# Kernel tuning notes

Measured on AMD Instinct MI355X. Metric: run time of the kernel, lower is better.

Reference implementation:

```python
import jax, jax.numpy as jnp
import numpy as np

B, S, T = 256, 1024, 64

def setup_inputs() -> dict:
    key = jax.random.key(0)
    k1, k2, k3, k4, k5 = jax.random.split(key, 5)
    emissions = jax.random.normal(k1, (B, S, T), dtype=jnp.float32)
    tags = jax.random.randint(k2, (B, S), 0, T, dtype=jnp.int64)
    mask = jnp.ones((B, S), dtype=jnp.int32)
    transitions = jax.random.normal(k3, (T, T), dtype=jnp.float32) * 0.1
    start_transitions = jax.random.normal(k4, (T,), dtype=jnp.float32) * 0.1
    end_transitions = jax.random.normal(k5, (T,), dtype=jnp.float32) * 0.1
    return {"emissions": emissions, "tags": tags, "mask": mask,
            "transitions": transitions, "start_transitions": start_transitions,
            "end_transitions": end_transitions}


def _gold_score(emissions, tags, maskf, transitions, start_transitions, end_transitions):
    # emission score at each gold tag: [B, S]
    emit = jnp.take_along_axis(emissions, tags[:, :, None], axis=2)[:, :, 0]
    # transition score between consecutive gold tags: [B, S-1]
    trans = transitions[tags[:, :-1], tags[:, 1:]]
    score = start_transitions[tags[:, 0]] + emit[:, 0]
    score = score + jnp.sum((trans + emit[:, 1:]) * maskf[:, 1:], axis=1)
    last_pos = maskf.astype(jnp.int32).sum(axis=1) - 1           # [B]
    last_tags = jnp.take_along_axis(tags, last_pos[:, None], axis=1)[:, 0]
    return score + end_transitions[last_tags]


def _log_partition(emissions, maskf, transitions, start_transitions, end_transitions):
    alpha0 = start_transitions[None, :] + emissions[:, 0]        # [B, T]

    def step(alpha, xs):
        emit_t, m_t = xs                                         # [B, T], [B]
        # scores[b, i, j] = alpha[b, i] + transitions[i, j] + emit_t[b, j]
        scores = alpha[:, :, None] + transitions[None, :, :] + emit_t[:, None, :]
        new_alpha = jax.nn.logsumexp(scores, axis=1)             # [B, T]
        alpha = jnp.where(m_t[:, None] > 0, new_alpha, alpha)
        return alpha, None

    xs = (jnp.swapaxes(emissions[:, 1:], 0, 1), jnp.swapaxes(maskf[:, 1:], 0, 1))
    alpha, _ = jax.lax.scan(step, alpha0, xs)
    return jax.nn.logsumexp(alpha + end_transitions[None, :], axis=1)  # [B]


def reference(emissions, tags, mask, transitions, start_transitions, end_transitions):
    maskf = mask.astype(emissions.dtype)
    log_Z = _log_partition(emissions, maskf, transitions, start_transitions, end_transitions)
    score = _gold_score(emissions, tags, maskf, transitions, start_transitions, end_transitions)
    return jnp.mean(log_Z - score)
```

## Files before the change

### kernel.cpp

```cpp
#include <hip/hip_runtime.h>

#define Bn 256
#define Sn 1024
#define Tn 64
#define NCH 16
#define BURN 64
#define SLAB 4
#define CROW 72
#define MROW 129
#define LN2 0.69314718055994531f
#define L7LN2 4.8520302639196169f

typedef __attribute__((ext_vector_type(8))) short short8;
typedef __attribute__((ext_vector_type(4))) float f32x4;

__device__ __forceinline__ unsigned short f2bf_rne(float f) {
  unsigned u = __float_as_uint(f);
  u = (u + 0x7fffu + ((u >> 16) & 1u)) >> 16;
  return (unsigned short)u;
}
__device__ __forceinline__ unsigned pk2(float hi, float lo) {
  return __builtin_amdgcn_perm(__float_as_uint(hi), __float_as_uint(lo), 0x07060302);
}
__device__ __forceinline__ unsigned pke(float a, float b) {
  return (unsigned)f2bf_rne(__expf(a - L7LN2)) |
         ((unsigned)f2bf_rne(__expf(b - L7LN2)) << 16);
}
__device__ __forceinline__ short8 cat4(uint2 a, uint2 b) {
  union { unsigned u[4]; short8 s; } x;
  x.u[0] = a.x; x.u[1] = a.y; x.u[2] = b.x; x.u[3] = b.y;
  return x.s;
}
__device__ __forceinline__ void gl_lds4(const void* src, void* dst) {
  __builtin_amdgcn_global_load_lds(
      (const __attribute__((address_space(1))) void*)src,
      (__attribute__((address_space(3))) void*)dst, 4, 0, 0);
}

__global__ __launch_bounds__(256, 1) void crf_scan(
    const float* __restrict__ em, const int* __restrict__ tags,
    const int* __restrict__ mask, const float* __restrict__ trans,
    const float* __restrict__ startt, const float* __restrict__ endt,
    float* __restrict__ wsL, float* __restrict__ wsGold,
    int* __restrict__ wsM, float* __restrict__ wsSE, float* __restrict__ wsA,
    int* __restrict__ cnt, float* __restrict__ out) {
  const int g = blockIdx.x & 15;
  const int c = blockIdx.x >> 4;
  const int Wc = (c == 0) ? 0 : BURN;
  const int Lc = (c == NCH - 1) ? 63 : 64;
  const int TOT = Wc + Lc;
  const int NSLAB = (TOT + SLAB - 1) / SLAB;
  const int t0 = 64 * c + 1;
  const int tstart = t0 - Wc;
  const int tid = threadIdx.x;
  const int wid = tid >> 6;
  const int lane = tid & 63;
  const int m = lane & 15;
  const int q = lane >> 4;
  const int mrow = 8 * (m >> 2) + (m & 3);

  __shared__ __align__(16) short convS[2][SLAB * 16 * CROW];
  __shared__ int maskL[16 * MROW];
  __shared__ int lastF;
  __shared__ float eend[64];
  __shared__ float rsum[4];

  short8 a00, a01, a10, a11, a20, a21, a30, a31;
  uint2 st0, st1, st2, st3;
  float Slog = 0.f;
  int K = 0, NL = 0;
  const f32x4 zero4 = {0.f, 0.f, 0.f, 0.f};

  const int mm_ = lane & 15, seg_ = lane >> 4;
  const int base_ = (seg_ >> 1) * 32 + (seg_ & 1) * 8;
  const size_t rowoff = (size_t)(16 * g + mm_) * Sn;
  const int ua = (wid == 1) ? 0 : 2;
  float4 A0, A1, A2, A3, A4, A5, A6, A7;
  float4 B0, B1, B2, B3, B4, B5, B6, B7;
  float4 C0, C1, C2, C3, C4, C5, C6, C7;
  float4 D0, D1, D2, D3, D4, D5, D6, D7;

#define LOADS(P, s) do { if ((s) < NSLAB) { \
    int ta_ = tstart + 4 * (s) + ua;  int tb_ = ta_ + 1; \
    ta_ = min(ta_, Sn - 1);  tb_ = min(tb_, Sn - 1);    \
    const float* pa_ = em + (rowoff + ta_) * 64 + seg_ * 16; \
    const float* pb_ = em + (rowoff + tb_) * 64 + seg_ * 16; \
    P##0 = *(const float4*)(pa_);      P##1 = *(const float4*)(pa_ + 4); \
    P##2 = *(const float4*)(pa_ + 8);  P##3 = *(const float4*)(pa_ + 12); \
    P##4 = *(const float4*)(pb_);      P##5 = *(const float4*)(pb_ + 4); \
    P##6 = *(const float4*)(pb_ + 8);  P##7 = *(const float4*)(pb_ + 12); } } while (0)

#define CONVW(P, s) do { if ((s) < NSLAB) { \
    short* cb_ = convS[(s) & 1]; \
    uint4 o0_, o1_; \
    o0_.x = pke((P##0).x, (P##0).y); o0_.y = pke((P##0).z, (P##0).w); \
    o1_.x = pke((P##1).x, (P##1).y); o1_.y = pke((P##1).z, (P##1).w); \
    o0_.z = pke((P##2).x, (P##2).y); o0_.w = pke((P##2).z, (P##2).w); \
    o1_.z = pke((P##3).x, (P##3).y); o1_.w = pke((P##3).z, (P##3).w); \
    short* cw_ = cb_ + (ua * 16 + mm_) * CROW + base_; \
    *(uint4*)(cw_) = o0_;  *(uint4*)(cw_ + 16) = o1_; \
    o0_.x = pke((P##4).x, (P##4).y); o0_.y = pke((P##4).z, (P##4).w); \
    o1_.x = pke((P##5).x, (P##5).y); o1_.y = pke((P##5).z, (P##5).w); \
    o0_.z = pke((P##6).x, (P##6).y); o0_.w = pke((P##6).z, (P##6).w); \
    o1_.z = pke((P##7).x, (P##7).y); o1_.w = pke((P##7).z, (P##7).w); \
    cw_ = cb_ + ((ua + 1) * 16 + mm_) * CROW + base_; \
    *(uint4*)(cw_) = o0_;  *(uint4*)(cw_ + 16) = o1_; } } while (0)

  if (wid == 0) {
#define LOADA(tm, kc, dst) { \
    _Pragma("unroll") for (int jj = 0; jj < 8; ++jj) { \
      int kk = kc * 32 + q * 8 + jj; \
      dst[jj] = (short)f2bf_rne(__expf(trans[kk * Tn + (32 * ((tm) >> 1) + 4 * ((tm) & 1) + mrow)])); \
    } }
    LOADA(0, 0, a00) LOADA(0, 1, a01) LOADA(1, 0, a10) LOADA(1, 1, a11)
    LOADA(2, 0, a20) LOADA(2, 1, a21) LOADA(3, 0, a30) LOADA(3, 1, a31)
#undef LOADA
    if (c == 0) {
#define INIT0(off, ss) { \
      float4 sv = *(const float4*)(startt + (off)); \
      float4 ev = *(const float4*)(em + (size_t)(16 * g + m) * Sn * Tn + (off)); \
      ss.x = (unsigned)f2bf_rne(__expf(sv.x + ev.x)) | \
             ((unsigned)f2bf_rne(__expf(sv.y + ev.y)) << 16); \
      ss.y = (unsigned)f2bf_rne(__expf(sv.z + ev.z)) | \
             ((unsigned)f2bf_rne(__expf(sv.w + ev.w)) << 16); }
      INIT0(8 * q, st0) INIT0(8 * q + 4, st1)
      INIT0(32 + 8 * q, st2) INIT0(36 + 8 * q, st3)
#undef INIT0
    } else {
      st0.x = 0x3F803F80u; st0.y = 0x3F803F80u; st1 = st0; st2 = st0; st3 = st0;
    }
  } else if (wid == 3) {
    for (int mm = 0; mm < 16; ++mm) {
      gl_lds4(mask + (size_t)(16 * g + mm) * Sn + tstart + lane,
              (void*)(maskL + mm * MROW));
      bool special = (c == NCH - 1) && (g == 15) && (mm == 15);
      if (!special)
        gl_lds4(mask + (size_t)(16 * g + mm) * Sn + tstart + 64 + lane,
                (void*)(maskL + mm * MROW + 64));
    }
    {
      const int bm = 16 * g + m;
      const int* tg = tags + (size_t)bm * Sn;
      const int* mkb = mask + (size_t)bm * Sn;
      const float* emb = em + (size_t)bm * Sn * Tn;
      float acc = 0.f;
      int cntg = 0;
      #pragma unroll 4
      for (int i = 0; i < 16; ++i) {
        int t = t0 + q + 4 * i;
        bool ok = t < t0 + Lc;
        int ts = ok ? t : t0;
        int mv = mkb[ts];
        int tp = tg[ts - 1], tc = tg[ts];
        float w = trans[tp * Tn + tc] + emb[(size_t)ts * Tn + tc];
        acc += (ok && mv) ? w : 0.f;
        cntg += ok ? mv : 0;
      }
      acc += __shfl_xor(acc, 16); acc += __shfl_xor(acc, 32);
      cntg += __shfl_xor(cntg, 16); cntg += __shfl_xor(cntg, 32);
      if (q == 0) { wsGold[c * 256 + bm] = acc; wsM[c * 256 + bm] = cntg; }
    }
    if (c == NCH - 1 && g == 15) {
      int t = tstart + 64 + lane;
      if (t < Sn) maskL[15 * MROW + 64 + lane] = mask[(size_t)255 * Sn + t];
    }
    asm volatile("s_waitcnt vmcnt(0) lgkmcnt(0)" ::: "memory");
  } else {
    LOADS(A, 0);
    LOADS(B, 1);
    LOADS(C, 2);
    LOADS(D, 3);
    CONVW(A, 0);
    asm volatile("s_waitcnt lgkmcnt(0)" ::: "memory");
  }
  __builtin_amdgcn_s_barrier();
  asm volatile("" ::: "memory");

#define UNP(ss, x0, x1, x2, x3) \
  x0 = __uint_as_float(ss.x << 16); x1 = __uint_as_float(ss.x & 0xffff0000u); \
  x2 = __uint_as_float(ss.y << 16); x3 = __uint_as_float(ss.y & 0xffff0000u);

  auto renorm = [&](int ttz) {
    float x00, x01, x02, x03, x10, x11, x12, x13;
    float x20, x21, x22, x23, x30, x31, x32, x33;
    UNP(st0, x00, x01, x02, x03) UNP(st1, x10, x11, x12, x13)
    UNP(st2, x20, x21, x22, x23) UNP(st3, x30, x31, x32, x33)
    float sm = (((x00 + x01) + (x02 + x03)) + ((x10 + x11) + (x12 + x13)))
             + (((x20 + x21) + (x22 + x23)) + ((x30 + x31) + (x32 + x33)));
    sm += __shfl_xor(sm, 16); sm += __shfl_xor(sm, 32);
    if (c != 0 && ttz == BURN) { Slog = __logf(sm); K = 0; NL = 0; }
    int k = 127 - (int)((__float_as_uint(sm) >> 23) & 255u);
    float fk = __uint_as_float((unsigned)(127 + k) << 23);
    x00 *= fk; x01 *= fk; x02 *= fk; x03 *= fk;
    x10 *= fk; x11 *= fk; x12 *= fk; x13 *= fk;
    x20 *= fk; x21 *= fk; x22 *= fk; x23 *= fk;
    x30 *= fk; x31 *= fk; x32 *= fk; x33 *= fk;
    st0.x = pk2(x01, x00); st0.y = pk2(x03, x02);
    st1.x = pk2(x11, x10); st1.y = pk2(x13, x12);
    st2.x = pk2(x21, x20); st2.y = pk2(x23, x22);
    st3.x = pk2(x31, x30); st3.y = pk2(x33, x32);
    K += k;
  };

  auto scan_step = [&](const short* ep, int tt) {
    uint2 eu0 = *(const uint2*)(ep + 0 + 4 * q);
    uint2 eu1 = *(const uint2*)(ep + 16 + 4 * q);
    uint2 eu2 = *(const uint2*)(ep + 32 + 4 * q);
    uint2 eu3 = *(const uint2*)(ep + 48 + 4 * q);
    int mv = maskL[m * MROW + tt];
    short8 b0 = cat4(st0, st1);
    short8 b1 = cat4(st2, st3);
    f32x4 d0 = __builtin_amdgcn_mfma_f32_16x16x32_bf16(a00, b0, zero4, 0, 0, 0);
    f32x4 d1 = __builtin_amdgcn_mfma_f32_16x16x32_bf16(a10, b0, zero4, 0, 0, 0);
    f32x4 d2 = __builtin_amdgcn_mfma_f32_16x16x32_bf16(a20, b0, zero4, 0, 0, 0);
    f32x4 d3 = __builtin_amdgcn_mfma_f32_16x16x32_bf16(a30, b0, zero4, 0, 0, 0);
    d0 = __builtin_amdgcn_mfma_f32_16x16x32_bf16(a01, b1, d0, 0, 0, 0);
    d1 = __builtin_amdgcn_mfma_f32_16x16x32_bf16(a11, b1, d1, 0, 0, 0);
    d2 = __builtin_amdgcn_mfma_f32_16x16x32_bf16(a21, b1, d2, 0, 0, 0);
    d3 = __builtin_amdgcn_mfma_f32_16x16x32_bf16(a31, b1, d3, 0, 0, 0);
    const bool live = (mv != 0);
#define EPI(dd, eu, ss) { \
    float e0 = __uint_as_float(eu.x << 16); \
    float e1 = __uint_as_float(eu.x & 0xffff0000u); \
    float e2 = __uint_as_float(eu.y << 16); \
    float e3 = __uint_as_float(eu.y & 0xffff0000u); \
    unsigned nx = pk2(dd[1] * e1, dd[0] * e0); \
    unsigned ny = pk2(dd[3] * e3, dd[2] * e2); \
    ss.x = live ? nx : ss.x; \
    ss.y = live ? ny : ss.y; }
    EPI(d0, eu0, st0) EPI(d1, eu1, st1) EPI(d2, eu2, st2) EPI(d3, eu3, st3)
#undef EPI
    NL += (live && tt >= Wc) ? 1 : 0;
  };

  const int RT = (TOT - 4) >> 2;
  for (int r = 0; r < NSLAB; ++r) {
    if (wid == 0) {
      if ((r & 1) == 0) renorm(4 * r);
      const short* cbase = convS[r & 1];
      if (r < RT) {
        #pragma unroll
        for (int u = 0; u < SLAB; ++u)
          scan_step(cbase + (u * 16 + m) * CROW, 4 * r + u);
      } else {
        #pragma unroll
        for (int u = 0; u < SLAB; ++u)
          if (4 * r + u < TOT)
            scan_step(cbase + (u * 16 + m) * CROW, 4 * r + u);
      }
    } else if (wid == 1 || wid == 2) {
      switch (r & 3) {
        case 0: LOADS(A, r + 4); CONVW(B, r + 1); break;
        case 1: LOADS(B, r + 4); CONVW(C, r + 1); break;
        case 2: LOADS(C, r + 4); CONVW(D, r + 1); break;
        default: LOADS(D, r + 4); CONVW(A, r + 1); break;
      }
      asm volatile("s_waitcnt lgkmcnt(0)" ::: "memory");
    }
    __builtin_amdgcn_s_barrier();
    asm volatile("" ::: "memory");
  }
#undef LOADS
#undef CONVW

  if (wid == 0) {
    float x00, x01, x02, x03, x10, x11, x12, x13;
    float x20, x21, x22, x23, x30, x31, x32, x33;
    UNP(st0, x00, x01, x02, x03) UNP(st1, x10, x11, x12, x13)
    UNP(st2, x20, x21, x22, x23) UNP(st3, x30, x31, x32, x33)
    float sm = (((x00 + x01) + (x02 + x03)) + ((x10 + x11) + (x12 + x13)))
             + (((x20 + x21) + (x22 + x23)) + ((x30 + x31) + (x32 + x33)));
    sm += __shfl_xor(sm, 16); sm += __shfl_xor(sm, 32);
    const int bm = 16 * g + m;
    float L = __logf(sm) - Slog + LN2 * (float)(7 * NL - K);
    if (q == 0) wsL[c * 256 + bm] = L;
    if (c == NCH - 1) {
      if (q == 0) wsSE[bm] = __logf(sm);
      wsA[(8 * q + 0) * 256 + bm] = x00;  wsA[(8 * q + 1) * 256 + bm] = x01;
      wsA[(8 * q + 2) * 256 + bm] = x02;  wsA[(8 * q + 3) * 256 + bm] = x03;
      wsA[(8 * q + 4) * 256 + bm] = x10;  wsA[(8 * q + 5) * 256 + bm] = x11;
      wsA[(8 * q + 6) * 256 + bm] = x12;  wsA[(8 * q + 7) * 256 + bm] = x13;
      wsA[(32 + 8 * q + 0) * 256 + bm] = x20; wsA[(32 + 8 * q + 1) * 256 + bm] = x21;
      wsA[(32 + 8 * q + 2) * 256 + bm] = x22; wsA[(32 + 8 * q + 3) * 256 + bm] = x23;
      wsA[(36 + 8 * q + 0) * 256 + bm] = x30; wsA[(36 + 8 * q + 1) * 256 + bm] = x31;
      wsA[(36 + 8 * q + 2) * 256 + bm] = x32; wsA[(36 + 8 * q + 3) * 256 + bm] = x33;
    }
  }
#undef UNP

  __threadfence();
  __syncthreads();
  if (tid == 0) lastF = (atomicAdd(cnt, 1) == 255) ? 1 : 0;
  __syncthreads();
  if (lastF) {
    __threadfence();
    if (tid < 64) eend[tid] = __expf(endt[tid]);
    __syncthreads();
    float vsum = 0.f;
    for (int bb = tid; bb < Bn; bb += 256) {
      float sumL = 0.f, gold = 0.f;
      int msum = 0;
      #pragma unroll
      for (int cc = 0; cc < NCH; ++cc) {
        sumL += wsL[cc * 256 + bb];
        gold += wsGold[cc * 256 + bb];
        msum += wsM[cc * 256 + bb];
      }
      msum += mask[(size_t)bb * Sn];
      float se = 0.f;
      for (int jj = 0; jj < Tn; ++jj) se += wsA[jj * 256 + bb] * eend[jj];
      float logZ = sumL + __logf(se) - wsSE[bb];
      int tg0 = tags[(size_t)bb * Sn];
      int lastTag = tags[(size_t)bb * Sn + (msum - 1)];
      gold += startt[tg0] + em[(size_t)bb * Sn * Tn + tg0] + endt[lastTag];
      vsum += logZ - gold;
    }
    #pragma unroll
    for (int o = 32; o > 0; o >>= 1) vsum += __shfl_xor(vsum, o, 64);
    if (lane == 0) rsum[wid] = vsum;
    __syncthreads();
    if (tid == 0) out[0] = (rsum[0] + rsum[1] + rsum[2] + rsum[3]) * (1.0f / Bn);
  }
}

extern "C" void kernel_launch(void* const* d_in, const int* in_sizes, int n_in,
                              void* d_out, int out_size, void* d_ws, size_t ws_size,
                              hipStream_t stream) {
  const float* em     = (const float*)d_in[0];
  const int*   tags   = (const int*)d_in[1];
  const int*   mask   = (const int*)d_in[2];
  const float* trans  = (const float*)d_in[3];
  const float* startt = (const float*)d_in[4];
  const float* endt   = (const float*)d_in[5];
  float* out = (float*)d_out;

  float* wsL    = (float*)d_ws;
  float* wsGold = wsL + NCH * 256;
  int*   wsM    = (int*)(wsGold + NCH * 256);
  float* wsSE   = (float*)(wsM + NCH * 256);
  float* wsA    = wsSE + 256;
  int*   cnt    = (int*)(wsA + 64 * 256);

  hipMemsetAsync(cnt, 0, sizeof(int), stream);
  crf_scan<<<256, 256, 0, stream>>>(em, tags, mask, trans, startt, endt,
                                    wsL, wsGold, wsM, wsSE, wsA, cnt, out);
}
```

Before: 165.1 us.

## Split each block to eight batch rows and launch twice as many blocks

Each workgroup now handles 8 batch rows instead of 16, and the grid doubles to 512 blocks with launch bounds allowing two blocks per CU. The 16-row MFMA still runs, with lanes 8-15 duplicating rows 0-7 and their outputs masked. This aims to fill more of the GPU's CUs and shorten each block's serial chain of loads and conversions. In exchange half of the MFMA work is redundant, and register limits under two blocks per CU may cause spills.

```diff
diff --git a/kernel.cpp b/kernel.cpp
--- a/kernel.cpp
+++ b/kernel.cpp
@@ -4,6 +4,7 @@
 #define Sn 1024
 #define Tn 64
 #define NCH 16
+#define NGRP 32
 #define BURN 64
 #define SLAB 4
 #define CROW 72
@@ -37,15 +38,15 @@
       (__attribute__((address_space(3))) void*)dst, 4, 0, 0);
 }
 
-__global__ __launch_bounds__(256, 1) void crf_scan(
+__global__ __launch_bounds__(256, 2) void crf_scan(
     const float* __restrict__ em, const int* __restrict__ tags,
     const int* __restrict__ mask, const float* __restrict__ trans,
     const float* __restrict__ startt, const float* __restrict__ endt,
     float* __restrict__ wsL, float* __restrict__ wsGold,
     int* __restrict__ wsM, float* __restrict__ wsSE, float* __restrict__ wsA,
     int* __restrict__ cnt, float* __restrict__ out) {
-  const int g = blockIdx.x & 15;
-  const int c = blockIdx.x >> 4;
+  const int g = blockIdx.x & 31;
+  const int c = blockIdx.x >> 5;
   const int Wc = (c == 0) ? 0 : BURN;
   const int Lc = (c == NCH - 1) ? 63 : 64;
   const int TOT = Wc + Lc;
@@ -57,10 +58,11 @@
   const int lane = tid & 63;
   const int m = lane & 15;
   const int q = lane >> 4;
+  const int r8 = m & 7;
   const int mrow = 8 * (m >> 2) + (m & 3);
 
-  __shared__ __align__(16) short convS[2][SLAB * 16 * CROW];
-  __shared__ int maskL[16 * MROW];
+  __shared__ __align__(16) short convS[2][SLAB * 8 * CROW];
+  __shared__ int maskL[8 * MROW];
   __shared__ int lastF;
   __shared__ float eend[64];
   __shared__ float rsum[4];
@@ -71,40 +73,34 @@
   int K = 0, NL = 0;
   const f32x4 zero4 = {0.f, 0.f, 0.f, 0.f};
 
-  const int mm_ = lane & 15, seg_ = lane >> 4;
-  const int base_ = (seg_ >> 1) * 32 + (seg_ & 1) * 8;
-  const size_t rowoff = (size_t)(16 * g + mm_) * Sn;
+  const int mm8_ = lane & 7, seg8_ = lane >> 3;
+  const int pos0_ = 32 * (seg8_ >> 2) + 4 * (seg8_ & 3);
+  const size_t rowoff = (size_t)(8 * g + mm8_) * Sn;
   const int ua = (wid == 1) ? 0 : 2;
-  float4 A0, A1, A2, A3, A4, A5, A6, A7;
-  float4 B0, B1, B2, B3, B4, B5, B6, B7;
-  float4 C0, C1, C2, C3, C4, C5, C6, C7;
-  float4 D0, D1, D2, D3, D4, D5, D6, D7;
+  float4 A0, A1, A2, A3;
+  float4 B0, B1, B2, B3;
+  float4 C0, C1, C2, C3;
+  float4 D0, D1, D2, D3;
 
 #define LOADS(P, s) do { if ((s) < NSLAB) { \
     int ta_ = tstart + 4 * (s) + ua;  int tb_ = ta_ + 1; \
     ta_ = min(ta_, Sn - 1);  tb_ = min(tb_, Sn - 1);    \
-    const float* pa_ = em + (rowoff + ta_) * 64 + seg_ * 16; \
-    const float* pb_ = em + (rowoff + tb_) * 64 + seg_ * 16; \
+    const float* pa_ = em + (rowoff + ta_) * 64 + 8 * seg8_; \
+    const float* pb_ = em + (rowoff + tb_) * 64 + 8 * seg8_; \
     P##0 = *(const float4*)(pa_);      P##1 = *(const float4*)(pa_ + 4); \
-    P##2 = *(const float4*)(pa_ + 8);  P##3 = *(const float4*)(pa_ + 12); \
-    P##4 = *(const float4*)(pb_);      P##5 = *(const float4*)(pb_ + 4); \
-    P##6 = *(const float4*)(pb_ + 8);  P##7 = *(const float4*)(pb_ + 12); } } while (0)
+    P##2 = *(const float4*)(pb_);      P##3 = *(const float4*)(pb_ + 4); } } while (0)
 
 #define CONVW(P, s) do { if ((s) < NSLAB) { \
     short* cb_ = convS[(s) & 1]; \
-    uint4 o0_, o1_; \
-    o0_.x = pke((P##0).x, (P##0).y); o0_.y = pke((P##0).z, (P##0).w); \
-    o1_.x = pke((P##1).x, (P##1).y); o1_.y = pke((P##1).z, (P##1).w); \
-    o0_.z = pke((P##2).x, (P##2).y); o0_.w = pke((P##2).z, (P##2).w); \
-    o1_.z = pke((P##3).x, (P##3).y); o1_.w = pke((P##3).z, (P##3).w); \
-    short* cw_ = cb_ + (ua * 16 + mm_) * CROW + base_; \
-    *(uint4*)(cw_) = o0_;  *(uint4*)(cw_ + 16) = o1_; \
-    o0_.x = pke((P##4).x, (P##4).y); o0_.y = pke((P##4).z, (P##4).w); \
-    o1_.x = pke((P##5).x, (P##5).y); o1_.y = pke((P##5).z, (P##5).w); \
-    o0_.z = pke((P##6).x, (P##6).y); o0_.w = pke((P##6).z, (P##6).w); \
-    o1_.z = pke((P##7).x, (P##7).y); o1_.w = pke((P##7).z, (P##7).w); \
-    cw_ = cb_ + ((ua + 1) * 16 + mm_) * CROW + base_; \
-    *(uint4*)(cw_) = o0_;  *(uint4*)(cw_ + 16) = o1_; } } while (0)
+    uint2 w0_, w1_; \
+    w0_.x = pke((P##0).x, (P##0).y); w0_.y = pke((P##0).z, (P##0).w); \
+    w1_.x = pke((P##1).x, (P##1).y); w1_.y = pke((P##1).z, (P##1).w); \
+    short* cw_ = cb_ + (ua * 8 + mm8_) * CROW + pos0_; \
+    *(uint2*)(cw_) = w0_;  *(uint2*)(cw_ + 16) = w1_; \
+    w0_.x = pke((P##2).x, (P##2).y); w0_.y = pke((P##2).z, (P##2).w); \
+    w1_.x = pke((P##3).x, (P##3).y); w1_.y = pke((P##3).z, (P##3).w); \
+    cw_ = cb_ + ((ua + 1) * 8 + mm8_) * CROW + pos0_; \
+    *(uint2*)(cw_) = w0_;  *(uint2*)(cw_ + 16) = w1_; } } while (0)
 
   if (wid == 0) {
 #define LOADA(tm, kc, dst) { \
@@ -118,7 +114,7 @@
     if (c == 0) {
 #define INIT0(off, ss) { \
       float4 sv = *(const float4*)(startt + (off)); \
-      float4 ev = *(const float4*)(em + (size_t)(16 * g + m) * Sn * Tn + (off)); \
+      float4 ev = *(const float4*)(em + (size_t)(8 * g + r8) * Sn * Tn + (off)); \
       ss.x = (unsigned)f2bf_rne(__expf(sv.x + ev.x)) | \
              ((unsigned)f2bf_rne(__expf(sv.y + ev.y)) << 16); \
       ss.y = (unsigned)f2bf_rne(__expf(sv.z + ev.z)) | \
@@ -130,16 +126,16 @@
       st0.x = 0x3F803F80u; st0.y = 0x3F803F80u; st1 = st0; st2 = st0; st3 = st0;
     }
   } else if (wid == 3) {
-    for (int mm = 0; mm < 16; ++mm) {
-      gl_lds4(mask + (size_t)(16 * g + mm) * Sn + tstart + lane,
+    for (int mm = 0; mm < 8; ++mm) {
+      gl_lds4(mask + (size_t)(8 * g + mm) * Sn + tstart + lane,
               (void*)(maskL + mm * MROW));
-      bool special = (c == NCH - 1) && (g == 15) && (mm == 15);
+      bool special = (c == NCH - 1) && (g == NGRP - 1) && (mm == 7);
       if (!special)
-        gl_lds4(mask + (size_t)(16 * g + mm) * Sn + tstart + 64 + lane,
+        gl_lds4(mask + (size_t)(8 * g + mm) * Sn + tstart + 64 + lane,
                 (void*)(maskL + mm * MROW + 64));
     }
     {
-      const int bm = 16 * g + m;
+      const int bm = 8 * g + r8;
       const int* tg = tags + (size_t)bm * Sn;
       const int* mkb = mask + (size_t)bm * Sn;
       const float* emb = em + (size_t)bm * Sn * Tn;
@@ -158,11 +154,11 @@
       }
       acc += __shfl_xor(acc, 16); acc += __shfl_xor(acc, 32);
       cntg += __shfl_xor(cntg, 16); cntg += __shfl_xor(cntg, 32);
-      if (q == 0) { wsGold[c * 256 + bm] = acc; wsM[c * 256 + bm] = cntg; }
-    }
-    if (c == NCH - 1 && g == 15) {
+      if (q == 0 && m < 8) { wsGold[c * 256 + bm] = acc; wsM[c * 256 + bm] = cntg; }
+    }
+    if (c == NCH - 1 && g == NGRP - 1) {
       int t = tstart + 64 + lane;
-      if (t < Sn) maskL[15 * MROW + 64 + lane] = mask[(size_t)255 * Sn + t];
+      if (t < Sn) maskL[7 * MROW + 64 + lane] = mask[(size_t)255 * Sn + t];
     }
     asm volatile("s_waitcnt vmcnt(0) lgkmcnt(0)" ::: "memory");
   } else {
@@ -207,7 +203,7 @@
     uint2 eu1 = *(const uint2*)(ep + 16 + 4 * q);
     uint2 eu2 = *(const uint2*)(ep + 32 + 4 * q);
     uint2 eu3 = *(const uint2*)(ep + 48 + 4 * q);
-    int mv = maskL[m * MROW + tt];
+    int mv = maskL[r8 * MROW + tt];
     short8 b0 = cat4(st0, st1);
     short8 b1 = cat4(st2, st3);
     f32x4 d0 = __builtin_amdgcn_mfma_f32_16x16x32_bf16(a00, b0, zero4, 0, 0, 0);
@@ -241,12 +237,12 @@
       if (r < RT) {
         #pragma unroll
         for (int u = 0; u < SLAB; ++u)
-          scan_step(cbase + (u * 16 + m) * CROW, 4 * r + u);
+          scan_step(cbase + (u * 8 + r8) * CROW, 4 * r + u);
       } else {
         #pragma unroll
         for (int u = 0; u < SLAB; ++u)
           if (4 * r + u < TOT)
-            scan_step(cbase + (u * 16 + m) * CROW, 4 * r + u);
+            scan_step(cbase + (u * 8 + r8) * CROW, 4 * r + u);
       }
     } else if (wid == 1 || wid == 2) {
       switch (r & 3) {
@@ -271,10 +267,10 @@
     float sm = (((x00 + x01) + (x02 + x03)) + ((x10 + x11) + (x12 + x13)))
              + (((x20 + x21) + (x22 + x23)) + ((x30 + x31) + (x32 + x33)));
     sm += __shfl_xor(sm, 16); sm += __shfl_xor(sm, 32);
-    const int bm = 16 * g + m;
+    const int bm = 8 * g + r8;
     float L = __logf(sm) - Slog + LN2 * (float)(7 * NL - K);
-    if (q == 0) wsL[c * 256 + bm] = L;
-    if (c == NCH - 1) {
+    if (q == 0 && m < 8) wsL[c * 256 + bm] = L;
+    if (c == NCH - 1 && m < 8) {
       if (q == 0) wsSE[bm] = __logf(sm);
       wsA[(8 * q + 0) * 256 + bm] = x00;  wsA[(8 * q + 1) * 256 + bm] = x01;
       wsA[(8 * q + 2) * 256 + bm] = x02;  wsA[(8 * q + 3) * 256 + bm] = x03;
@@ -290,7 +286,7 @@
 
   __threadfence();
   __syncthreads();
-  if (tid == 0) lastF = (atomicAdd(cnt, 1) == 255) ? 1 : 0;
+  if (tid == 0) lastF = (atomicAdd(cnt, 1) == 511) ? 1 : 0;
   __syncthreads();
   if (lastF) {
     __threadfence();
@@ -342,6 +338,6 @@
   int*   cnt    = (int*)(wsA + 64 * 256);
 
   hipMemsetAsync(cnt, 0, sizeof(int), stream);
-  crf_scan<<<256, 256, 0, stream>>>(em, tags, mask, trans, startt, endt,
+  crf_scan<<<512, 256, 0, stream>>>(em, tags, mask, trans, startt, endt,
                                     wsL, wsGold, wsM, wsSE, wsA, cnt, out);
 }
```

After: 183.1 us. 10.9% more time.

## Split exp/bf16 emission conversion into a prep kernel and DMA-pipeline the scan

Applied to the files above, without the earlier changes.

Adds a prep kernel that turns the whole emission tensor into exp-scaled bf16 in a swizzled layout stored in workspace. The scan kernel then uses 128 threads: one wave runs the MFMA recurrence and the other streams precomputed slabs into a four-deep LDS ring with direct global-to-LDS loads. This removes the in-loop conversion work and the register-staged loads from the critical path. The cost is an extra full pass over emissions (read fp32, write bf16) plus a second launch. The old kernel is kept as a fallback for when the workspace is too small.

```diff
diff --git a/kernel.cpp b/kernel.cpp
--- a/kernel.cpp
+++ b/kernel.cpp
@@ -31,13 +31,299 @@
   x.u[0] = a.x; x.u[1] = a.y; x.u[2] = b.x; x.u[3] = b.y;
   return x.s;
 }
+__device__ __forceinline__ void gl_lds16(const void* src, void* dst) {
+  __builtin_amdgcn_global_load_lds(
+      (const __attribute__((address_space(1))) void*)src,
+      (__attribute__((address_space(3))) void*)dst, 16, 0, 0);
+}
 __device__ __forceinline__ void gl_lds4(const void* src, void* dst) {
   __builtin_amdgcn_global_load_lds(
       (const __attribute__((address_space(1))) void*)src,
       (__attribute__((address_space(3))) void*)dst, 4, 0, 0);
 }
 
-__global__ __launch_bounds__(256, 1) void crf_scan(
+__global__ __launch_bounds__(256) void crf_prep(const float* __restrict__ em,
+                                                short* __restrict__ em2) {
+  int idx = blockIdx.x * 256 + threadIdx.x;
+  if (idx >= Bn * Sn * 4) return;
+  const int cell = idx >> 2;
+  const int j = idx & 3;
+  const int b = cell >> 10;
+  const float* src = em + (size_t)cell * 64;
+  float4 v0 = *(const float4*)(src + 8 * j);
+  float4 v1 = *(const float4*)(src + 8 * j + 4);
+  float4 v2 = *(const float4*)(src + 32 + 8 * j);
+  float4 v3 = *(const float4*)(src + 32 + 8 * j + 4);
+  uint4 O1, O2;
+  O1.x = pke(v0.x, v0.y); O1.y = pke(v0.z, v0.w);
+  O1.z = pke(v1.x, v1.y); O1.w = pke(v1.z, v1.w);
+  O2.x = pke(v2.x, v2.y); O2.y = pke(v2.z, v2.w);
+  O2.z = pke(v3.x, v3.y); O2.w = pke(v3.z, v3.w);
+  short* dst = em2 + (size_t)cell * 64;
+  const int sw = (b & 7) << 3;
+  *(uint4*)(dst + ((j * 16) ^ sw)) = O1;
+  *(uint4*)(dst + ((j * 16 + 8) ^ sw)) = O2;
+}
+
+__global__ __launch_bounds__(128, 1) void crf_scan2(
+    const float* __restrict__ em, const int* __restrict__ tags,
+    const int* __restrict__ mask, const float* __restrict__ trans,
+    const float* __restrict__ startt, const float* __restrict__ endt,
+    const short* __restrict__ em2,
+    float* __restrict__ wsL, float* __restrict__ wsGold,
+    int* __restrict__ wsM, float* __restrict__ wsSE, float* __restrict__ wsA,
+    int* __restrict__ cnt, float* __restrict__ out) {
+  const int g = blockIdx.x & 15;
+  const int c = blockIdx.x >> 4;
+  const int Wc = (c == 0) ? 0 : BURN;
+  const int Lc = (c == NCH - 1) ? 63 : 64;
+  const int TOT = Wc + Lc;
+  const int NSLAB = (TOT + SLAB - 1) / SLAB;
+  const int t0 = 64 * c + 1;
+  const int tstart = t0 - Wc;
+  const int tid = threadIdx.x;
+  const int wid = tid >> 6;
+  const int lane = tid & 63;
+  const int m = lane & 15;
+  const int q = lane >> 4;
+  const int mrow = 8 * (m >> 2) + (m & 3);
+  const int swm = (m & 7) << 3;
+  const int hi = lane >> 3, inner = lane & 7;
+
+  __shared__ __align__(16) short ring[4][SLAB * 16 * 64];
+  __shared__ int maskL[16 * MROW];
+  __shared__ int lastF;
+  __shared__ float eend[64];
+  __shared__ float rsum[2];
+
+  short8 a00, a01, a10, a11, a20, a21, a30, a31;
+  uint2 st0, st1, st2, st3;
+  float Slog = 0.f;
+  int K = 0, NL = 0;
+  const f32x4 zero4 = {0.f, 0.f, 0.f, 0.f};
+
+  auto issue_slab = [&](int s) {
+    if (s >= NSLAB) return;
+    short* dstb = ring[s & 3];
+    const int rem = min(SLAB, TOT - 4 * s);
+    const int Ts = tstart + 4 * s;
+    for (int u = 0; u < rem; ++u)
+      for (int hf = 0; hf < 2; ++hf)
+        gl_lds16(em2 + ((size_t)(16 * g + hf * 8 + hi) * Sn + (Ts + u)) * 64 + inner * 8,
+                 dstb + (u * 16 + hf * 8) * 64);
+  };
+
+  if (wid == 0) {
+#define LOADA(tm, kc, dst) { \
+    _Pragma("unroll") for (int jj = 0; jj < 8; ++jj) { \
+      int kk = kc * 32 + q * 8 + jj; \
+      dst[jj] = (short)f2bf_rne(__expf(trans[kk * Tn + (32 * ((tm) >> 1) + 4 * ((tm) & 1) + mrow)])); \
+    } }
+    LOADA(0, 0, a00) LOADA(0, 1, a01) LOADA(1, 0, a10) LOADA(1, 1, a11)
+    LOADA(2, 0, a20) LOADA(2, 1, a21) LOADA(3, 0, a30) LOADA(3, 1, a31)
+#undef LOADA
+    if (c == 0) {
+#define INIT0(off, ss) { \
+      float4 sv = *(const float4*)(startt + (off)); \
+      float4 ev = *(const float4*)(em + (size_t)(16 * g + m) * Sn * Tn + (off)); \
+      ss.x = (unsigned)f2bf_rne(__expf(sv.x + ev.x)) | \
+             ((unsigned)f2bf_rne(__expf(sv.y + ev.y)) << 16); \
+      ss.y = (unsigned)f2bf_rne(__expf(sv.z + ev.z)) | \
+             ((unsigned)f2bf_rne(__expf(sv.w + ev.w)) << 16); }
+      INIT0(8 * q, st0) INIT0(8 * q + 4, st1)
+      INIT0(32 + 8 * q, st2) INIT0(36 + 8 * q, st3)
+#undef INIT0
+    } else {
+      st0.x = 0x3F803F80u; st0.y = 0x3F803F80u; st1 = st0; st2 = st0; st3 = st0;
+    }
+    if (c == NCH - 1 && g == 15) {
+      int t = tstart + 64 + lane;
+      if (t < Sn) maskL[15 * MROW + 64 + lane] = mask[(size_t)255 * Sn + t];
+    }
+    asm volatile("s_waitcnt vmcnt(0) lgkmcnt(0)" ::: "memory");
+  } else {
+    for (int mm = 0; mm < 16; ++mm) {
+      gl_lds4(mask + (size_t)(16 * g + mm) * Sn + tstart + lane,
+              (void*)(maskL + mm * MROW));
+      bool special = (c == NCH - 1) && (g == 15) && (mm == 15);
+      if (!special)
+        gl_lds4(mask + (size_t)(16 * g + mm) * Sn + tstart + 64 + lane,
+                (void*)(maskL + mm * MROW + 64));
+    }
+    {
+      const int bm = 16 * g + m;
+      const int* tg = tags + (size_t)bm * Sn;
+      const int* mkb = mask + (size_t)bm * Sn;
+      const float* emb = em + (size_t)bm * Sn * Tn;
+      float acc = 0.f;
+      int cntg = 0;
+      #pragma unroll 4
+      for (int i = 0; i < 16; ++i) {
+        int t = t0 + q + 4 * i;
+        bool ok = t < t0 + Lc;
+        int ts = ok ? t : t0;
+        int mv = mkb[ts];
+        int tp = tg[ts - 1], tc = tg[ts];
+        float w = trans[tp * Tn + tc] + emb[(size_t)ts * Tn + tc];
+        acc += (ok && mv) ? w : 0.f;
+        cntg += ok ? mv : 0;
+      }
+      acc += __shfl_xor(acc, 16); acc += __shfl_xor(acc, 32);
+      cntg += __shfl_xor(cntg, 16); cntg += __shfl_xor(cntg, 32);
+      if (q == 0) { wsGold[c * 256 + bm] = acc; wsM[c * 256 + bm] = cntg; }
+    }
+    asm volatile("s_waitcnt vmcnt(0)" ::: "memory");
+    issue_slab(0); issue_slab(1); issue_slab(2);
+    asm volatile("s_waitcnt vmcnt(16)" ::: "memory");
+  }
+  __builtin_amdgcn_s_barrier();
+  asm volatile("" ::: "memory");
+
+#define UNP(ss, x0, x1, x2, x3) \
+  x0 = __uint_as_float(ss.x << 16); x1 = __uint_as_float(ss.x & 0xffff0000u); \
+  x2 = __uint_as_float(ss.y << 16); x3 = __uint_as_float(ss.y & 0xffff0000u);
+
+  auto renorm = [&](int ttz) {
+    float x00, x01, x02, x03, x10, x11, x12, x13;
+    float x20, x21, x22, x23, x30, x31, x32, x33;
+    UNP(st0, x00, x01, x02, x03) UNP(st1, x10, x11, x12, x13)
+    UNP(st2, x20, x21, x22, x23) UNP(st3, x30, x31, x32, x33)
+    float sm = (((x00 + x01) + (x02 + x03)) + ((x10 + x11) + (x12 + x13)))
+             + (((x20 + x21) + (x22 + x23)) + ((x30 + x31) + (x32 + x33)));
+    sm += __shfl_xor(sm, 16); sm += __shfl_xor(sm, 32);
+    if (c != 0 && ttz == BURN) { Slog = __logf(sm); K = 0; NL = 0; }
+    int k = 127 - (int)((__float_as_uint(sm) >> 23) & 255u);
+    float fk = __uint_as_float((unsigned)(127 + k) << 23);
+    x00 *= fk; x01 *= fk; x02 *= fk; x03 *= fk;
+    x10 *= fk; x11 *= fk; x12 *= fk; x13 *= fk;
+    x20 *= fk; x21 *= fk; x22 *= fk; x23 *= fk;
+    x30 *= fk; x31 *= fk; x32 *= fk; x33 *= fk;
+    st0.x = pk2(x01, x00); st0.y = pk2(x03, x02);
+    st1.x = pk2(x11, x10); st1.y = pk2(x13, x12);
+    st2.x = pk2(x21, x20); st2.y = pk2(x23, x22);
+    st3.x = pk2(x31, x30); st3.y = pk2(x33, x32);
+    K += k;
+  };
+
+  auto scan_step = [&](const short* cellb, int tt) {
+    uint4 E01 = *(const uint4*)(cellb + ((q * 16) ^ swm));
+    uint4 E23 = *(const uint4*)(cellb + ((q * 16 + 8) ^ swm));
+    uint2 eu0; eu0.x = E01.x; eu0.y = E01.y;
+    uint2 eu1; eu1.x = E01.z; eu1.y = E01.w;
+    uint2 eu2; eu2.x = E23.x; eu2.y = E23.y;
+    uint2 eu3; eu3.x = E23.z; eu3.y = E23.w;
+    int mv = maskL[m * MROW + tt];
+    short8 b0 = cat4(st0, st1);
+    short8 b1 = cat4(st2, st3);
+    f32x4 d0 = __builtin_amdgcn_mfma_f32_16x16x32_bf16(a00, b0, zero4, 0, 0, 0);
+    f32x4 d1 = __builtin_amdgcn_mfma_f32_16x16x32_bf16(a10, b0, zero4, 0, 0, 0);
+    f32x4 d2 = __builtin_amdgcn_mfma_f32_16x16x32_bf16(a20, b0, zero4, 0, 0, 0);
+    f32x4 d3 = __builtin_amdgcn_mfma_f32_16x16x32_bf16(a30, b0, zero4, 0, 0, 0);
+    d0 = __builtin_amdgcn_mfma_f32_16x16x32_bf16(a01, b1, d0, 0, 0, 0);
+    d1 = __builtin_amdgcn_mfma_f32_16x16x32_bf16(a11, b1, d1, 0, 0, 0);
+    d2 = __builtin_amdgcn_mfma_f32_16x16x32_bf16(a21, b1, d2, 0, 0, 0);
+    d3 = __builtin_amdgcn_mfma_f32_16x16x32_bf16(a31, b1, d3, 0, 0, 0);
+    const bool live = (mv != 0);
+#define EPI(dd, eu, ss) { \
+    float e0 = __uint_as_float(eu.x << 16); \
+    float e1 = __uint_as_float(eu.x & 0xffff0000u); \
+    float e2 = __uint_as_float(eu.y << 16); \
+    float e3 = __uint_as_float(eu.y & 0xffff0000u); \
+    unsigned nx = pk2(dd[1] * e1, dd[0] * e0); \
+    unsigned ny = pk2(dd[3] * e3, dd[2] * e2); \
+    ss.x = live ? nx : ss.x; \
+    ss.y = live ? ny : ss.y; }
+    EPI(d0, eu0, st0) EPI(d1, eu1, st1) EPI(d2, eu2, st2) EPI(d3, eu3, st3)
+#undef EPI
+    NL += (live && tt >= Wc) ? 1 : 0;
+  };
+
+  const int RT = (TOT - 4) >> 2;
+  for (int r = 0; r < NSLAB; ++r) {
+    if (wid == 0) {
+      if ((r & 1) == 0) renorm(4 * r);
+      const short* rb = ring[r & 3];
+      if (r < RT) {
+        #pragma unroll
+        for (int u = 0; u < SLAB; ++u)
+          scan_step(rb + (u * 16 + m) * 64, 4 * r + u);
+      } else {
+        #pragma unroll
+        for (int u = 0; u < SLAB; ++u)
+          if (4 * r + u < TOT)
+            scan_step(rb + (u * 16 + m) * 64, 4 * r + u);
+      }
+    } else {
+      issue_slab(r + 3);
+      if (r + 3 < NSLAB)      asm volatile("s_waitcnt vmcnt(14)" ::: "memory");
+      else if (r + 2 < NSLAB) asm volatile("s_waitcnt vmcnt(6)" ::: "memory");
+      else                    asm volatile("s_waitcnt vmcnt(0)" ::: "memory");
+    }
+    __builtin_amdgcn_s_barrier();
+    asm volatile("" ::: "memory");
+  }
+
+  if (wid == 0) {
+    float x00, x01, x02, x03, x10, x11, x12, x13;
+    float x20, x21, x22, x23, x30, x31, x32, x33;
+    UNP(st0, x00, x01, x02, x03) UNP(st1, x10, x11, x12, x13)
+    UNP(st2, x20, x21, x22, x23) UNP(st3, x30, x31, x32, x33)
+    float sm = (((x00 + x01) + (x02 + x03)) + ((x10 + x11) + (x12 + x13)))
+             + (((x20 + x21) + (x22 + x23)) + ((x30 + x31) + (x32 + x33)));
+    sm += __shfl_xor(sm, 16); sm += __shfl_xor(sm, 32);
+    const int bm = 16 * g + m;
+    float L = __logf(sm) - Slog + LN2 * (float)(7 * NL - K);
+    if (q == 0) wsL[c * 256 + bm] = L;
+    if (c == NCH - 1) {
+      if (q == 0) wsSE[bm] = __logf(sm);
+      wsA[(8 * q + 0) * 256 + bm] = x00;  wsA[(8 * q + 1) * 256 + bm] = x01;
+      wsA[(8 * q + 2) * 256 + bm] = x02;  wsA[(8 * q + 3) * 256 + bm] = x03;
+      wsA[(8 * q + 4) * 256 + bm] = x10;  wsA[(8 * q + 5) * 256 + bm] = x11;
+      wsA[(8 * q + 6) * 256 + bm] = x12;  wsA[(8 * q + 7) * 256 + bm] = x13;
+      wsA[(32 + 8 * q + 0) * 256 + bm] = x20; wsA[(32 + 8 * q + 1) * 256 + bm] = x21;
+      wsA[(32 + 8 * q + 2) * 256 + bm] = x22; wsA[(32 + 8 * q + 3) * 256 + bm] = x23;
+      wsA[(36 + 8 * q + 0) * 256 + bm] = x30; wsA[(36 + 8 * q + 1) * 256 + bm] = x31;
+      wsA[(36 + 8 * q + 2) * 256 + bm] = x32; wsA[(36 + 8 * q + 3) * 256 + bm] = x33;
+    }
+  }
+#undef UNP
+
+  __threadfence();
+  __syncthreads();
+  if (tid == 0) lastF = (atomicAdd(cnt, 1) == 255) ? 1 : 0;
+  __syncthreads();
+  if (lastF) {
+    __threadfence();
+    if (tid < 64) eend[tid] = __expf(endt[tid]);
+    __syncthreads();
+    float vsum = 0.f;
+    for (int bb = tid; bb < Bn; bb += 128) {
+      float sumL = 0.f, gold = 0.f;
+      int msum = 0;
+      #pragma unroll
+      for (int cc = 0; cc < NCH; ++cc) {
+        sumL += wsL[cc * 256 + bb];
+        gold += wsGold[cc * 256 + bb];
+        msum += wsM[cc * 256 + bb];
+      }
+      msum += mask[(size_t)bb * Sn];
+      float se = 0.f;
+      for (int jj = 0; jj < Tn; ++jj) se += wsA[jj * 256 + bb] * eend[jj];
+      float logZ = sumL + __logf(se) - wsSE[bb];
+      int tg0 = tags[(size_t)bb * Sn];
+      int lastTag = tags[(size_t)bb * Sn + (msum - 1)];
+      gold += startt[tg0] + em[(size_t)bb * Sn * Tn + tg0] + endt[lastTag];
+      vsum += logZ - gold;
+    }
+    #pragma unroll
+    for (int o = 32; o > 0; o >>= 1) vsum += __shfl_xor(vsum, o, 64);
+    if (lane == 0) rsum[wid] = vsum;
+    __syncthreads();
+    if (tid == 0) out[0] = (rsum[0] + rsum[1]) * (1.0f / Bn);
+  }
+}
+
+__global__ __launch_bounds__(256, 1) void crf_scan_fb(
     const float* __restrict__ em, const int* __restrict__ tags,
     const int* __restrict__ mask, const float* __restrict__ trans,
     const float* __restrict__ startt, const float* __restrict__ endt,
@@ -82,7 +368,7 @@
 
 #define LOADS(P, s) do { if ((s) < NSLAB) { \
     int ta_ = tstart + 4 * (s) + ua;  int tb_ = ta_ + 1; \
-    ta_ = min(ta_, Sn - 1);  tb_ = min(tb_, Sn - 1);    \
+    ta_ = min(ta_, Sn - 1);  tb_ = min(tb_, Sn - 1); \
     const float* pa_ = em + (rowoff + ta_) * 64 + seg_ * 16; \
     const float* pb_ = em + (rowoff + tb_) * 64 + seg_ * 16; \
     P##0 = *(const float4*)(pa_);      P##1 = *(const float4*)(pa_ + 4); \
@@ -341,7 +627,18 @@
   float* wsA    = wsSE + 256;
   int*   cnt    = (int*)(wsA + 64 * 256);
 
+  size_t off = (size_t)((char*)(cnt + 1) - (char*)d_ws);
+  off = (off + 255) & ~(size_t)255;
+  short* em2 = (short*)((char*)d_ws + off);
+  const size_t need = off + (size_t)Bn * Sn * Tn * sizeof(short);
+
   hipMemsetAsync(cnt, 0, sizeof(int), stream);
-  crf_scan<<<256, 256, 0, stream>>>(em, tags, mask, trans, startt, endt,
-                                    wsL, wsGold, wsM, wsSE, wsA, cnt, out);
-}
+  if (ws_size >= need) {
+    crf_prep<<<4096, 256, 0, stream>>>(em, em2);
+    crf_scan2<<<256, 128, 0, stream>>>(em, tags, mask, trans, startt, endt, em2,
+                                       wsL, wsGold, wsM, wsSE, wsA, cnt, out);
+  } else {
+    crf_scan_fb<<<256, 256, 0, stream>>>(em, tags, mask, trans, startt, endt,
+                                         wsL, wsGold, wsM, wsSE, wsA, cnt, out);
+  }
+}
```

Result: no change. 168.4 us (+2.0%).
